# Optimization experiments

Hardware: AMD Instinct MI355X
Metric: run time of the kernel (lower is better)

The kernel has to match this reference:

```python
import jax, jax.numpy as jnp
import numpy as np

B, S, D, H = 1, 512, 128, 128
EPS = 1e-5


def layernorm(x, g, b):
    mu = jnp.mean(x, axis=-1, keepdims=True)
    var = jnp.mean(jnp.square(x - mu), axis=-1, keepdims=True)
    return (x - mu) * jax.lax.rsqrt(var + EPS) * g + b


def setup_inputs() -> dict:
    key = jax.random.key(0)
    ks = jax.random.split(key, 10)
    scale_d = 1.0 / np.sqrt(D)
    scale_h = 1.0 / np.sqrt(H)
    return {
        "x": jax.random.normal(ks[0], (B, S, S, D), dtype=jnp.float32),
        "mask": jax.random.uniform(ks[1], (B, S, S), dtype=jnp.float32),
        "norm_g": jnp.ones((D,), jnp.float32),
        "norm_b": jnp.zeros((D,), jnp.float32),
        "Wl": jax.random.normal(ks[2], (H, D), jnp.float32) * scale_d,
        "Wr": jax.random.normal(ks[3], (H, D), jnp.float32) * scale_d,
        "Wlg": jax.random.normal(ks[4], (H, D), jnp.float32) * scale_d,
        "Wrg": jax.random.normal(ks[5], (H, D), jnp.float32) * scale_d,
        "Wog": jax.random.normal(ks[6], (H, D), jnp.float32) * scale_d,
        "out_norm_g": jnp.ones((H,), jnp.float32),
        "out_norm_b": jnp.zeros((H,), jnp.float32),
        "Wout": jax.random.normal(ks[7], (D, H), jnp.float32) * scale_h,
    }


def reference(x, mask, norm_g, norm_b, Wl, Wr, Wlg, Wrg, Wog, out_norm_g, out_norm_b, Wout):
    # x: [B,S,S,D], mask: [B,S,S]
    xn = layernorm(x, norm_g, norm_b)
    m = mask[..., None]  # [B,S,S,1]
    left = (xn @ Wl.T) * m * jax.nn.sigmoid(xn @ Wlg.T)   # [B,S,S,H]
    right = (xn @ Wr.T) * m * jax.nn.sigmoid(xn @ Wrg.T)  # [B,S,S,H]
    out_gate = jax.nn.sigmoid(xn @ Wog.T)                  # [B,S,S,H]
    # per-channel triangular contraction over k
    out = jnp.einsum('bikd,bjkd->bijd', left, right)       # [B,S,S,H]
    out = layernorm(out, out_norm_g, out_norm_b) * out_gate
    return out @ Wout.T  # [B,S,S,D]
```

## Files before the change

kernel.cpp:

```cpp
#include <hip/hip_runtime.h>
#include <hip/hip_bf16.h>
#include <cstdint>

typedef unsigned short u16;
typedef unsigned int   u32;
typedef __bf16 bf16x8 __attribute__((ext_vector_type(8)));
typedef float  f32x4  __attribute__((ext_vector_type(4)));

#define S_    512
#define D_    128
#define H_    128
#define NPOS_ (S_ * S_)
#define LN_EPS 1e-5f

__device__ __forceinline__ u16 f2bf(float f) {
  union { __hip_bfloat16 h; u16 u; } cv;
  cv.h = __float2bfloat16(f);
  return cv.u;
}
__device__ __forceinline__ float bflo(u32 p) { return __uint_as_float(p << 16); }
__device__ __forceinline__ float bfhi(u32 p) { return __uint_as_float(p & 0xffff0000u); }
__device__ __forceinline__ float sigmoidf_(float x) { return 1.f / (1.f + __expf(-x)); }

__device__ __forceinline__ void gld16(const void* g, void* l) {
  __builtin_amdgcn_global_load_lds(
      (const __attribute__((address_space(1))) void*)g,
      (__attribute__((address_space(3))) void*)l, 16, 0, 0);
}

template <int CPR, int TOTAL, int SWZ>
__device__ __forceinline__ void stage_tile(const char* gbase, int ld_bytes, char* lds, int tid) {
#pragma unroll
  for (int c = tid; c < TOTAL; c += 256) {
    int row = c / CPR;
    int col = c - row * CPR;
    int scol = col ^ (row & SWZ);
    gld16(gbase + (size_t)row * ld_bytes + (size_t)scol * 16, lds + (size_t)c * 16);
  }
}

__global__ __launch_bounds__(256) void k_prep(
    const float* __restrict__ wl, const float* __restrict__ wlg,
    const float* __restrict__ wr, const float* __restrict__ wrg,
    const float* __restrict__ wog, const float* __restrict__ wout,
    u16* __restrict__ wb) {
  int i = blockIdx.x * 256 + threadIdx.x;
  int m = i >> 14, o = i & 16383;
  const float* src = (m == 0) ? wl : (m == 1) ? wlg : (m == 2) ? wr
                   : (m == 3) ? wrg : (m == 4) ? wog : wout;
  wb[i] = f2bf(src[o]);
}

__device__ __forceinline__ void proj_k128(
    const u16* __restrict__ Wm, const u16* __restrict__ Wg,
    const u16* Xs, int wr, int wc, int quad, int lq,
    f32x4 acc0[4][4], f32x4 acc1[4][4]) {
#pragma unroll
  for (int ks = 0; ks < 4; ++ks) {
    const int kc = ks * 4 + quad;
    bf16x8 b[4], am[4], ag[4];
#pragma unroll
    for (int ni = 0; ni < 4; ++ni) {
      const int br = wc * 64 + ni * 16 + lq;
      b[ni] = *(const bf16x8*)((const char*)Xs + br * 256 + ((kc ^ (br & 15)) << 4));
    }
#pragma unroll
    for (int mi = 0; mi < 4; ++mi) {
      const int ar = wr * 64 + mi * 16 + lq;
      am[mi] = *(const bf16x8*)&Wm[(size_t)ar * D_ + kc * 8];
      if (Wg) ag[mi] = *(const bf16x8*)&Wg[(size_t)ar * D_ + kc * 8];
    }
#pragma unroll
    for (int mi = 0; mi < 4; ++mi)
#pragma unroll
      for (int ni = 0; ni < 4; ++ni) {
        acc0[mi][ni] = __builtin_amdgcn_mfma_f32_16x16x32_bf16(am[mi], b[ni], acc0[mi][ni], 0, 0, 0);
        if (Wg)
          acc1[mi][ni] = __builtin_amdgcn_mfma_f32_16x16x32_bf16(ag[mi], b[ni], acc1[mi][ni], 0, 0, 0);
      }
  }
}

__device__ __forceinline__ void ts_put(u16* T, int row, int col, u16 v) {
  *(u16*)((char*)T + row * 256 + ((((col >> 3) ^ (row & 15)) << 4) | ((col & 7) << 1))) = v;
}

__device__ __forceinline__ void ts_flush(const u16* T, u16* dst, size_t ld, size_t c0, int tid) {
#pragma unroll
  for (int it = 0; it < 8; ++it) {
    const int c = it * 256 + tid;
    const int row = c >> 4, cc = c & 15;
    bf16x8 v = *(const bf16x8*)((const char*)T + row * 256 + ((cc ^ (row & 15)) << 4));
    *(bf16x8*)&dst[(size_t)row * ld + c0 + cc * 8] = v;
  }
}

__global__ __launch_bounds__(256, 2) void k_lnproj(
    const float* __restrict__ x, const float* __restrict__ mask,
    const float* __restrict__ ng, const float* __restrict__ nb,
    const u16* __restrict__ wb, u16* __restrict__ left_t,
    u16* __restrict__ right_t, u16* __restrict__ gate_t) {
  __shared__ u16 Xs[128 * 128];
  __shared__ u16 Ts[128 * 128];
  const int tid = threadIdx.x, w = tid >> 6, l = tid & 63;
  const int r0 = blockIdx.x * 128;
  const int half = l >> 5, lh = l & 31;

  {
    const float4 gg = ((const float4*)ng)[lh];
    const float4 bb = ((const float4*)nb)[lh];
#pragma unroll 4
    for (int it = 0; it < 16; ++it) {
      const int rr = it * 8 + w * 2 + half;
      float4 v = ((const float4*)(x + (size_t)(r0 + rr) * D_))[lh];
      float s = v.x + v.y + v.z + v.w;
      float q = v.x * v.x + v.y * v.y + v.z * v.z + v.w * v.w;
#pragma unroll
      for (int off = 16; off >= 1; off >>= 1) {
        s += __shfl_xor(s, off);
        q += __shfl_xor(q, off);
      }
      const float mu  = s * (1.f / 128.f);
      const float var = q * (1.f / 128.f) - mu * mu;
      const float rs  = rsqrtf(var + LN_EPS);
      const u32 p0 = (u32)f2bf((v.x - mu) * rs * gg.x + bb.x)
                   | ((u32)f2bf((v.y - mu) * rs * gg.y + bb.y) << 16);
      const u32 p1 = (u32)f2bf((v.z - mu) * rs * gg.z + bb.z)
                   | ((u32)f2bf((v.w - mu) * rs * gg.w + bb.w) << 16);
      u32* d = (u32*)((char*)Xs + rr * 256 + ((((lh >> 1)) ^ (rr & 15)) << 4) + ((lh & 1) << 3));
      d[0] = p0;
      d[1] = p1;
    }
  }
  __syncthreads();

  const int wr = w >> 1, wc = w & 1, quad = l >> 4, lq = l & 15;
  const f32x4 vz = {0.f, 0.f, 0.f, 0.f};
  f32x4 acc0[4][4], acc1[4][4];

#pragma unroll
  for (int g = 0; g < 2; ++g) {
    const u16* Wm = wb + (size_t)(2 * g) * (H_ * D_);
    const u16* Wg = wb + (size_t)(2 * g + 1) * (H_ * D_);
    u16* dst = g ? right_t : left_t;
#pragma unroll
    for (int i = 0; i < 4; ++i)
#pragma unroll
      for (int j = 0; j < 4; ++j) { acc0[i][j] = vz; acc1[i][j] = vz; }

    proj_k128(Wm, Wg, Xs, wr, wc, quad, lq, acc0, acc1);

#pragma unroll
    for (int ni = 0; ni < 4; ++ni) {
      const int rc = wc * 64 + ni * 16 + lq;
      const float mk = mask[r0 + rc];
#pragma unroll
      for (int mi = 0; mi < 4; ++mi)
#pragma unroll
        for (int reg = 0; reg < 4; ++reg) {
          const int hrow = wr * 64 + mi * 16 + quad * 4 + reg;
          ts_put(Ts, hrow, rc, f2bf(acc0[mi][ni][reg] * mk * sigmoidf_(acc1[mi][ni][reg])));
        }
    }
    __syncthreads();
    ts_flush(Ts, dst, NPOS_, r0, tid);
    __syncthreads();
  }

#pragma unroll
  for (int i = 0; i < 4; ++i)
#pragma unroll
    for (int j = 0; j < 4; ++j) acc0[i][j] = vz;

  proj_k128(wb + (size_t)4 * (H_ * D_), (const u16*)nullptr, Xs, wr, wc, quad, lq, acc0, acc1);

#pragma unroll
  for (int ni = 0; ni < 4; ++ni) {
    const int rc = wc * 64 + ni * 16 + lq;
#pragma unroll
    for (int mi = 0; mi < 4; ++mi)
#pragma unroll
      for (int reg = 0; reg < 4; ++reg) {
        const int hrow = wr * 64 + mi * 16 + quad * 4 + reg;
        ts_put(Ts, hrow, rc, f2bf(sigmoidf_(acc0[mi][ni][reg])));
      }
  }
  __syncthreads();
  ts_flush(Ts, gate_t, NPOS_, r0, tid);
}

__global__ __launch_bounds__(256, 2) void k_einsum(
    const u16* __restrict__ left_t, const u16* __restrict__ right_t,
    u16* __restrict__ out_t) {
  const int d = blockIdx.x;
  const int t = blockIdx.y;
  const int i0 = (t >> 2) * 128, j0 = (t & 3) * 128;
  __shared__ u16 SM[128 * 128];
  u16* As = SM;
  u16* Bs = SM + 128 * 64;
  const u16* L = left_t + (size_t)d * NPOS_;
  const u16* R = right_t + (size_t)d * NPOS_;
  const int tid = threadIdx.x;
  const int w = tid >> 6, l = tid & 63;
  const int wr = w >> 1, wc = w & 1, quad = l >> 4, lq = l & 15;

  const f32x4 vz = {0.f, 0.f, 0.f, 0.f};
  f32x4 acc[4][4];
#pragma unroll
  for (int i = 0; i < 4; ++i)
#pragma unroll
    for (int j = 0; j < 4; ++j) acc[i][j] = vz;

  for (int kt = 0; kt < 8; ++kt) {
    stage_tile<8, 1024, 7>((const char*)L + ((size_t)i0 * S_ + kt * 64) * 2, S_ * 2, (char*)As, tid);
    stage_tile<8, 1024, 7>((const char*)R + ((size_t)j0 * S_ + kt * 64) * 2, S_ * 2, (char*)Bs, tid);
    __syncthreads();
#pragma unroll
    for (int kk = 0; kk < 2; ++kk) {
      const int cs = kk * 4 + quad;
      bf16x8 a[4], b[4];
#pragma unroll
      for (int mi = 0; mi < 4; ++mi) {
        const int row = wr * 64 + mi * 16 + lq;
        a[mi] = *(const bf16x8*)((const char*)As + row * 128 + ((cs ^ (row & 7)) << 4));
      }
#pragma unroll
      for (int ni = 0; ni < 4; ++ni) {
        const int row = wc * 64 + ni * 16 + lq;
        b[ni] = *(const bf16x8*)((const char*)Bs + row * 128 + ((cs ^ (row & 7)) << 4));
      }
#pragma unroll
      for (int mi = 0; mi < 4; ++mi)
#pragma unroll
        for (int ni = 0; ni < 4; ++ni)
          acc[mi][ni] = __builtin_amdgcn_mfma_f32_16x16x32_bf16(a[mi], b[ni], acc[mi][ni], 0, 0, 0);
    }
    __syncthreads();
  }

  u16* T = SM;
#pragma unroll
  for (int mi = 0; mi < 4; ++mi)
#pragma unroll
    for (int ni = 0; ni < 4; ++ni) {
      const int jc = wc * 64 + ni * 16 + lq;
#pragma unroll
      for (int reg = 0; reg < 4; ++reg) {
        const int row = wr * 64 + mi * 16 + quad * 4 + reg;
        ts_put(T, row, jc, f2bf(acc[mi][ni][reg]));
      }
    }
  __syncthreads();
  u16* O = out_t + (size_t)d * NPOS_ + (size_t)i0 * S_;
  ts_flush(T, O, S_, j0, tid);
}

__global__ __launch_bounds__(256, 2) void k_final(
    const u16* __restrict__ out_t, const u16* __restrict__ gate_t,
    const float* __restrict__ og, const float* __restrict__ ob,
    const u16* __restrict__ wout_b, float* __restrict__ out) {
  __shared__ u16 A_lds[128 * 136];
  __shared__ u16 Wlds[128 * 128];
  __shared__ float psum[4][128], pq[4][128];
  __shared__ float mu_s[128], rs_s[128];
  const int tid = threadIdx.x, w = tid >> 6, l = tid & 63;
  const int r0 = blockIdx.x * 128;

  stage_tile<16, 2048, 15>((const char*)wout_b, 256, (char*)Wlds, tid);

  float s0 = 0.f, s1 = 0.f, q0 = 0.f, q1 = 0.f;
  for (int it = 0; it < 32; ++it) {
    int d = it * 4 + w;
    u32 p = *(const u32*)&out_t[(size_t)d * NPOS_ + r0 + 2 * l];
    float f0 = bflo(p), f1 = bfhi(p);
    s0 += f0; s1 += f1; q0 += f0 * f0; q1 += f1 * f1;
  }
  psum[w][2 * l] = s0; psum[w][2 * l + 1] = s1;
  pq[w][2 * l] = q0;   pq[w][2 * l + 1] = q1;
  __syncthreads();
  if (tid < 128) {
    float s = psum[0][tid] + psum[1][tid] + psum[2][tid] + psum[3][tid];
    float q = pq[0][tid] + pq[1][tid] + pq[2][tid] + pq[3][tid];
    float mu  = s * (1.f / 128.f);
    float var = q * (1.f / 128.f) - mu * mu;
    mu_s[tid] = mu;
    rs_s[tid] = rsqrtf(var + LN_EPS);
  }
  __syncthreads();

  for (int it = 0; it < 32; ++it) {
    int d = it * 4 + w;
    u32 p  = *(const u32*)&out_t[(size_t)d * NPOS_ + r0 + 2 * l];
    u32 gp = *(const u32*)&gate_t[(size_t)d * NPOS_ + r0 + 2 * l];
    float gd = og[d], bd = ob[d];
    float f0 = bflo(p), f1 = bfhi(p);
    float g0 = bflo(gp), g1 = bfhi(gp);
    int ja = 2 * l, jb = 2 * l + 1;
    float a0 = ((f0 - mu_s[ja]) * rs_s[ja] * gd + bd) * g0;
    float a1 = ((f1 - mu_s[jb]) * rs_s[jb] * gd + bd) * g1;
    A_lds[(size_t)ja * 136 + d] = f2bf(a0);
    A_lds[(size_t)jb * 136 + d] = f2bf(a1);
  }
  __syncthreads();

  const int wr = w >> 1, wc = w & 1, quad = l >> 4, lq = l & 15;
  const f32x4 vz = {0.f, 0.f, 0.f, 0.f};
  f32x4 acc[4][4];
#pragma unroll
  for (int i = 0; i < 4; ++i)
#pragma unroll
    for (int j = 0; j < 4; ++j) acc[i][j] = vz;
#pragma unroll
  for (int kk = 0; kk < 4; ++kk) {
    const int ko = kk * 32 + quad * 8;
    const int cs = kk * 4 + quad;
    bf16x8 a[4], b[4];
#pragma unroll
    for (int mi = 0; mi < 4; ++mi)
      a[mi] = *(const bf16x8*)&A_lds[(wr * 64 + mi * 16 + lq) * 136 + ko];
#pragma unroll
    for (int ni = 0; ni < 4; ++ni) {
      const int row = wc * 64 + ni * 16 + lq;
      b[ni] = *(const bf16x8*)((const char*)Wlds + row * 256 + ((cs ^ (row & 15)) << 4));
    }
#pragma unroll
    for (int mi = 0; mi < 4; ++mi)
#pragma unroll
      for (int ni = 0; ni < 4; ++ni)
        acc[mi][ni] = __builtin_amdgcn_mfma_f32_16x16x32_bf16(a[mi], b[ni], acc[mi][ni], 0, 0, 0);
  }
  const int lc = lq;
#pragma unroll
  for (int mi = 0; mi < 4; ++mi)
#pragma unroll
    for (int ni = 0; ni < 4; ++ni) {
      const int dout = wc * 64 + ni * 16 + lc;
#pragma unroll
      for (int reg = 0; reg < 4; ++reg) {
        const int row = r0 + wr * 64 + mi * 16 + quad * 4 + reg;
        out[(size_t)row * D_ + dout] = acc[mi][ni][reg];
      }
    }
}

extern "C" void kernel_launch(void* const* d_in, const int* in_sizes, int n_in,
                              void* d_out, int out_size, void* d_ws, size_t ws_size,
                              hipStream_t stream) {
  const float* x    = (const float*)d_in[0];
  const float* mask = (const float*)d_in[1];
  const float* ng   = (const float*)d_in[2];
  const float* nb   = (const float*)d_in[3];
  const float* Wl   = (const float*)d_in[4];
  const float* Wr   = (const float*)d_in[5];
  const float* Wlg  = (const float*)d_in[6];
  const float* Wrg  = (const float*)d_in[7];
  const float* Wog  = (const float*)d_in[8];
  const float* og   = (const float*)d_in[9];
  const float* ob   = (const float*)d_in[10];
  const float* Wout = (const float*)d_in[11];
  float* out = (float*)d_out;

  const size_t SLAB = (size_t)NPOS_ * H_ * 2;
  char* ws = (char*)d_ws;
  u16* left_t  = (u16*)(ws + SLAB);
  u16* right_t = (u16*)(ws + 2 * SLAB);
  u16* gate_t  = (u16*)(ws + 3 * SLAB);
  u16* wb      = (u16*)(ws + 4 * SLAB);
  u16* out_t   = (u16*)(ws);
  if (ws_size < 4 * SLAB + 6 * H_ * D_ * sizeof(u16)) return;

  k_prep<<<384, 256, 0, stream>>>(Wl, Wlg, Wr, Wrg, Wog, Wout, wb);
  k_lnproj<<<2048, 256, 0, stream>>>(x, mask, ng, nb, wb, left_t, right_t, gate_t);
  k_einsum<<<dim3(128, 16), 256, 0, stream>>>(left_t, right_t, out_t);
  k_final<<<2048, 256, 0, stream>>>(out_t, gate_t, og, ob, wb + 5 * H_ * D_, out);
}
```

Baseline: 489.9 us.

## Drop LDS transpose staging in projection, split N tiles, remap einsum blocks per XCD

The projection kernel no longer stages outputs through a second 32KB LDS tile and flushes them. Instead it writes bf16 results straight to the transposed global arrays, processing the column tile in two 32-wide halves so the accumulator arrays shrink. Launch bounds are raised to 3 blocks per SM. Each direct store is a 2-byte write strided across 16-lane groups, which loses the coalesced 16-byte stores the flush used to provide. The einsum kernel also remaps its linear block index so that all tiles of one channel d land on the same XCD, which should improve L2 reuse of that channel's left/right planes.

```diff
diff --git a/kernel.cpp b/kernel.cpp
--- a/kernel.cpp
+++ b/kernel.cpp
@@ -51,17 +51,17 @@
   wb[i] = f2bf(src[o]);
 }
 
-__device__ __forceinline__ void proj_k128(
+__device__ __forceinline__ void proj_k64(
     const u16* __restrict__ Wm, const u16* __restrict__ Wg,
-    const u16* Xs, int wr, int wc, int quad, int lq,
-    f32x4 acc0[4][4], f32x4 acc1[4][4]) {
+    const u16* Xs, int wr, int rbase, int quad, int lq,
+    f32x4 acc0[4][2], f32x4 acc1[4][2]) {
 #pragma unroll
   for (int ks = 0; ks < 4; ++ks) {
     const int kc = ks * 4 + quad;
-    bf16x8 b[4], am[4], ag[4];
-#pragma unroll
-    for (int ni = 0; ni < 4; ++ni) {
-      const int br = wc * 64 + ni * 16 + lq;
+    bf16x8 b[2], am[4], ag[4];
+#pragma unroll
+    for (int ni = 0; ni < 2; ++ni) {
+      const int br = rbase + ni * 16 + lq;
       b[ni] = *(const bf16x8*)((const char*)Xs + br * 256 + ((kc ^ (br & 15)) << 4));
     }
 #pragma unroll
@@ -73,7 +73,7 @@
 #pragma unroll
     for (int mi = 0; mi < 4; ++mi)
 #pragma unroll
-      for (int ni = 0; ni < 4; ++ni) {
+      for (int ni = 0; ni < 2; ++ni) {
         acc0[mi][ni] = __builtin_amdgcn_mfma_f32_16x16x32_bf16(am[mi], b[ni], acc0[mi][ni], 0, 0, 0);
         if (Wg)
           acc1[mi][ni] = __builtin_amdgcn_mfma_f32_16x16x32_bf16(ag[mi], b[ni], acc1[mi][ni], 0, 0, 0);
@@ -81,27 +81,12 @@
   }
 }
 
-__device__ __forceinline__ void ts_put(u16* T, int row, int col, u16 v) {
-  *(u16*)((char*)T + row * 256 + ((((col >> 3) ^ (row & 15)) << 4) | ((col & 7) << 1))) = v;
-}
-
-__device__ __forceinline__ void ts_flush(const u16* T, u16* dst, size_t ld, size_t c0, int tid) {
-#pragma unroll
-  for (int it = 0; it < 8; ++it) {
-    const int c = it * 256 + tid;
-    const int row = c >> 4, cc = c & 15;
-    bf16x8 v = *(const bf16x8*)((const char*)T + row * 256 + ((cc ^ (row & 15)) << 4));
-    *(bf16x8*)&dst[(size_t)row * ld + c0 + cc * 8] = v;
-  }
-}
-
-__global__ __launch_bounds__(256, 2) void k_lnproj(
+__global__ __launch_bounds__(256, 3) void k_lnproj(
     const float* __restrict__ x, const float* __restrict__ mask,
     const float* __restrict__ ng, const float* __restrict__ nb,
     const u16* __restrict__ wb, u16* __restrict__ left_t,
     u16* __restrict__ right_t, u16* __restrict__ gate_t) {
   __shared__ u16 Xs[128 * 128];
-  __shared__ u16 Ts[128 * 128];
   const int tid = threadIdx.x, w = tid >> 6, l = tid & 63;
   const int r0 = blockIdx.x * 128;
   const int half = l >> 5, lh = l & 31;
@@ -136,7 +121,7 @@
 
   const int wr = w >> 1, wc = w & 1, quad = l >> 4, lq = l & 15;
   const f32x4 vz = {0.f, 0.f, 0.f, 0.f};
-  f32x4 acc0[4][4], acc1[4][4];
+  f32x4 acc0[4][2], acc1[4][2];
 
 #pragma unroll
   for (int g = 0; g < 2; ++g) {
@@ -144,56 +129,77 @@
     const u16* Wg = wb + (size_t)(2 * g + 1) * (H_ * D_);
     u16* dst = g ? right_t : left_t;
 #pragma unroll
+    for (int h = 0; h < 2; ++h) {
+      const int rbase = wc * 64 + h * 32;
+#pragma unroll
+      for (int i = 0; i < 4; ++i)
+#pragma unroll
+        for (int j = 0; j < 2; ++j) { acc0[i][j] = vz; acc1[i][j] = vz; }
+
+      proj_k64(Wm, Wg, Xs, wr, rbase, quad, lq, acc0, acc1);
+
+#pragma unroll
+      for (int ni = 0; ni < 2; ++ni) {
+        const int r = r0 + rbase + ni * 16 + lq;
+        const float mk = mask[r];
+#pragma unroll
+        for (int mi = 0; mi < 4; ++mi)
+#pragma unroll
+          for (int reg = 0; reg < 4; ++reg) {
+            const int hrow = wr * 64 + mi * 16 + quad * 4 + reg;
+            dst[(size_t)hrow * NPOS_ + r] =
+                f2bf(acc0[mi][ni][reg] * mk * sigmoidf_(acc1[mi][ni][reg]));
+          }
+      }
+    }
+  }
+
+#pragma unroll
+  for (int h = 0; h < 2; ++h) {
+    const int rbase = wc * 64 + h * 32;
+#pragma unroll
     for (int i = 0; i < 4; ++i)
 #pragma unroll
-      for (int j = 0; j < 4; ++j) { acc0[i][j] = vz; acc1[i][j] = vz; }
-
-    proj_k128(Wm, Wg, Xs, wr, wc, quad, lq, acc0, acc1);
-
-#pragma unroll
-    for (int ni = 0; ni < 4; ++ni) {
-      const int rc = wc * 64 + ni * 16 + lq;
-      const float mk = mask[r0 + rc];
+      for (int j = 0; j < 2; ++j) acc0[i][j] = vz;
+
+    proj_k64(wb + (size_t)4 * (H_ * D_), (const u16*)nullptr, Xs, wr, rbase, quad, lq, acc0, acc1);
+
+#pragma unroll
+    for (int ni = 0; ni < 2; ++ni) {
+      const int r = r0 + rbase + ni * 16 + lq;
 #pragma unroll
       for (int mi = 0; mi < 4; ++mi)
 #pragma unroll
         for (int reg = 0; reg < 4; ++reg) {
           const int hrow = wr * 64 + mi * 16 + quad * 4 + reg;
-          ts_put(Ts, hrow, rc, f2bf(acc0[mi][ni][reg] * mk * sigmoidf_(acc1[mi][ni][reg])));
+          gate_t[(size_t)hrow * NPOS_ + r] = f2bf(sigmoidf_(acc0[mi][ni][reg]));
         }
     }
-    __syncthreads();
-    ts_flush(Ts, dst, NPOS_, r0, tid);
-    __syncthreads();
-  }
-
-#pragma unroll
-  for (int i = 0; i < 4; ++i)
-#pragma unroll
-    for (int j = 0; j < 4; ++j) acc0[i][j] = vz;
-
-  proj_k128(wb + (size_t)4 * (H_ * D_), (const u16*)nullptr, Xs, wr, wc, quad, lq, acc0, acc1);
-
-#pragma unroll
-  for (int ni = 0; ni < 4; ++ni) {
-    const int rc = wc * 64 + ni * 16 + lq;
-#pragma unroll
-    for (int mi = 0; mi < 4; ++mi)
-#pragma unroll
-      for (int reg = 0; reg < 4; ++reg) {
-        const int hrow = wr * 64 + mi * 16 + quad * 4 + reg;
-        ts_put(Ts, hrow, rc, f2bf(sigmoidf_(acc0[mi][ni][reg])));
-      }
-  }
-  __syncthreads();
-  ts_flush(Ts, gate_t, NPOS_, r0, tid);
+  }
+}
+
+__device__ __forceinline__ void ts_put(u16* T, int row, int col, u16 v) {
+  *(u16*)((char*)T + row * 256 + ((((col >> 3) ^ (row & 15)) << 4) | ((col & 7) << 1))) = v;
+}
+
+__device__ __forceinline__ void ts_flush(const u16* T, u16* dst, size_t ld, size_t c0, int tid) {
+#pragma unroll
+  for (int it = 0; it < 8; ++it) {
+    const int c = it * 256 + tid;
+    const int row = c >> 4, cc = c & 15;
+    bf16x8 v = *(const bf16x8*)((const char*)T + row * 256 + ((cc ^ (row & 15)) << 4));
+    *(bf16x8*)&dst[(size_t)row * ld + c0 + cc * 8] = v;
+  }
 }
 
 __global__ __launch_bounds__(256, 2) void k_einsum(
     const u16* __restrict__ left_t, const u16* __restrict__ right_t,
     u16* __restrict__ out_t) {
-  const int d = blockIdx.x;
-  const int t = blockIdx.y;
+  const int lin  = blockIdx.y * (int)gridDim.x + blockIdx.x;
+  const int xcd  = lin & 7;
+  const int slot = lin >> 3;
+  const int d    = xcd * 16 + (slot >> 4);
+  const int t    = slot & 15;
   const int i0 = (t >> 2) * 128, j0 = (t & 3) * 128;
   __shared__ u16 SM[128 * 128];
   u16* As = SM;
@@ -329,12 +335,11 @@
       for (int ni = 0; ni < 4; ++ni)
         acc[mi][ni] = __builtin_amdgcn_mfma_f32_16x16x32_bf16(a[mi], b[ni], acc[mi][ni], 0, 0, 0);
   }
-  const int lc = lq;
 #pragma unroll
   for (int mi = 0; mi < 4; ++mi)
 #pragma unroll
     for (int ni = 0; ni < 4; ++ni) {
-      const int dout = wc * 64 + ni * 16 + lc;
+      const int dout = wc * 64 + ni * 16 + lq;
 #pragma unroll
       for (int reg = 0; reg < 4; ++reg) {
         const int row = r0 + wr * 64 + mi * 16 + quad * 4 + reg;
```

Result: slower. 668.2 us (+36.4%).
